# Performance work log

Hardware: AMD Instinct MI355X
Metric: run time of the kernel (lower is better)

The kernel has to match this reference:

```python
import jax, jax.numpy as jnp
import numpy as np

B, N, D_IN, D, H, L, NQ, NC, HID = 4, 25000, 32, 256, 8, 6, 100, 18, 1024


def _ln(x, g, b, eps=1e-5):
    m = jnp.mean(x, -1, keepdims=True)
    v = jnp.mean((x - m) ** 2, -1, keepdims=True)
    return (x - m) / jnp.sqrt(v + eps) * g + b


def _mha(q, kv, wqkv, bqkv, wo, bo, h):
    # q: (B, Lq, d), kv: (B, Lk, d); torch nn.MultiheadAttention math
    d = q.shape[-1]
    dh = d // h
    wq, wk, wv = jnp.split(wqkv, 3, axis=0)
    bq, bk, bv = jnp.split(bqkv, 3)
    Q = (q @ wq.T + bq).reshape(q.shape[0], q.shape[1], h, dh)
    K = (kv @ wk.T + bk).reshape(kv.shape[0], kv.shape[1], h, dh)
    V = (kv @ wv.T + bv).reshape(kv.shape[0], kv.shape[1], h, dh)
    s = jnp.einsum('bqhd,bkhd->bhqk', Q, K) / jnp.asarray(np.sqrt(dh), Q.dtype)
    a = jax.nn.softmax(s, axis=-1)
    o = jnp.einsum('bhqk,bkhd->bqhd', a, V).reshape(q.shape)
    return o @ wo.T + bo


def setup_inputs() -> dict:
    key = jax.random.key(0)
    ks = list(jax.random.split(key, 20))
    ki = iter(ks)

    def p(shape, s=0.02):
        return jax.random.normal(next(ki), shape, jnp.float32) * s

    inp = {
        'x': jax.random.normal(next(ki), (B * N, D_IN), jnp.float32),
        'batch_offsets': jnp.arange(B + 1, dtype=jnp.int32) * N,
        'ip_w': p((D, D_IN)), 'ip_b': jnp.zeros((D,), jnp.float32),
        'ip_ln_g': jnp.ones((D,), jnp.float32), 'ip_ln_b': jnp.zeros((D,), jnp.float32),
        'xm_w1': p((D, D_IN)), 'xm_b1': jnp.zeros((D,), jnp.float32),
        'xm_w2': p((D, D)), 'xm_b2': jnp.zeros((D,), jnp.float32),
        'query_embed': p((NQ, D), 1.0),
        'ca_wqkv': p((L, 3 * D, D)), 'ca_bqkv': jnp.zeros((L, 3 * D), jnp.float32),
        'ca_wo': p((L, D, D)), 'ca_bo': jnp.zeros((L, D), jnp.float32),
        'sa_wqkv': p((L, 3 * D, D)), 'sa_bqkv': jnp.zeros((L, 3 * D), jnp.float32),
        'sa_wo': p((L, D, D)), 'sa_bo': jnp.zeros((L, D), jnp.float32),
        'sa_ln_g': jnp.ones((L, D), jnp.float32), 'sa_ln_b': jnp.zeros((L, D), jnp.float32),
        'ffn_w1': p((L, HID, D)), 'ffn_b1': jnp.zeros((L, HID), jnp.float32),
        'ffn_w2': p((L, D, HID)), 'ffn_b2': jnp.zeros((L, D), jnp.float32),
        'ffn_ln_g': jnp.ones((L, D), jnp.float32), 'ffn_ln_b': jnp.zeros((L, D), jnp.float32),
        'out_ln_g': jnp.ones((D,), jnp.float32), 'out_ln_b': jnp.zeros((D,), jnp.float32),
        'cls_w1': p((D, D)), 'cls_b1': jnp.zeros((D,), jnp.float32),
        'cls_w2': p((NC + 1, D)), 'cls_b2': jnp.zeros((NC + 1,), jnp.float32),
    }
    return inp


def reference(x, batch_offsets, ip_w, ip_b, ip_ln_g, ip_ln_b, xm_w1, xm_b1, xm_w2, xm_b2,
              query_embed, ca_wqkv, ca_bqkv, ca_wo, ca_bo, sa_wqkv, sa_bqkv, sa_wo, sa_bo,
              sa_ln_g, sa_ln_b, ffn_w1, ffn_b1, ffn_w2, ffn_b2, ffn_ln_g, ffn_ln_b,
              out_ln_g, out_ln_b, cls_w1, cls_b1, cls_w2, cls_b2):
    b = batch_offsets.shape[0] - 1  # uniform segments -> batched attention
    n = x.shape[0] // b
    # input_proj: Linear -> LayerNorm -> ReLU
    inst = jax.nn.relu(_ln(x @ ip_w.T + ip_b, ip_ln_g, ip_ln_b)).reshape(b, n, -1)
    # x_mask: Linear -> ReLU -> Linear
    mask_feats = (jax.nn.relu(x @ xm_w1.T + xm_b1) @ xm_w2.T + xm_b2).reshape(b, n, -1)
    query = jnp.broadcast_to(query_embed, (b,) + query_embed.shape)
    for i in range(ca_wqkv.shape[0]):
        # CrossAttentionLayer: NOTE original discards dropout/norm results -> pure residual
        query = _mha(query, inst, ca_wqkv[i], ca_bqkv[i], ca_wo[i], ca_bo[i], H) + query
        # SelfAttentionLayer: residual + LayerNorm
        query = _ln(_mha(query, query, sa_wqkv[i], sa_bqkv[i], sa_wo[i], sa_bo[i], H) + query,
                    sa_ln_g[i], sa_ln_b[i])
        # FFN: residual + LayerNorm
        ff = jax.nn.relu(query @ ffn_w1[i].T + ffn_b1[i]) @ ffn_w2[i].T + ffn_b2[i]
        query = _ln(ff + query, ffn_ln_g[i], ffn_ln_b[i])
    qn = _ln(query, out_ln_g, out_ln_b)
    pred_labels = jax.nn.relu(qn @ cls_w1.T + cls_b1) @ cls_w2.T + cls_b2  # (b, NQ, NC+1)
    pred_masks = jnp.einsum('bqd,bnd->bqn', qn, mask_feats)  # (b, NQ, n)
    return pred_labels, pred_masks
```

## Files before the change

### kernel.cpp

```cpp
#include <hip/hip_runtime.h>

typedef unsigned short u16;
typedef unsigned int   u32;

constexpr int Bz   = 4;
constexpr int Ni   = 25000;
constexpr int BNi  = Bz * Ni;
constexpr int DIN  = 32;
constexpr int D    = 256;
constexpr int Hh   = 8;
constexpr int DH   = 32;
constexpr int Ll   = 6;
constexpr int NQ   = 100;
constexpr int NC1  = 19;
constexpr int HIDd = 1024;

constexpr int CHUNK  = 625;
constexpr int NCHUNK = Ni / CHUNK;
constexpr size_t PARTB = (size_t)Hh * NCHUNK * 128 * 34;
constexpr float SM_SCALE = 0.17677669529663687f;

__device__ __forceinline__ u16 f2b(float f) {
    union { float f; u32 u; } c; c.f = f;
    u32 u = c.u + 0x7FFFu + ((c.u >> 16) & 1u);
    return (u16)(u >> 16);
}

__global__ void k_cvt(const float* __restrict__ in, u16* __restrict__ out, int n) {
    for (int i = blockIdx.x * blockDim.x + threadIdx.x; i < n; i += gridDim.x * blockDim.x)
        out[i] = f2b(in[i]);
}

typedef __attribute__((ext_vector_type(8))) __bf16 bf8v;
typedef __attribute__((ext_vector_type(8))) short  s8v;
typedef __attribute__((ext_vector_type(4))) float  f4v;

template<bool DOLN>
__global__ __launch_bounds__(512) void k_inproj(
    const float* __restrict__ x, int row0, int Mloc,
    const u16* __restrict__ w16, const float* __restrict__ bias,
    const float* __restrict__ g, const float* __restrict__ bb,
    u16* __restrict__ outb)
{
    __shared__ u16 Ws[256 * 40];
    __shared__ float Cb[256], Cg[256], Cbb[256];
    const int tid = threadIdx.x, lane = tid & 63, w = tid >> 6;
    const int lr = lane & 15, hi = lane >> 4;

    for (int ch = tid; ch < 1024; ch += 512) {
        int r = ch >> 2, g4 = ch & 3;
        *(uint4*)&Ws[r * 40 + g4 * 8] = *(const uint4*)(w16 + r * 32 + g4 * 8);
    }
    if (tid < 256) {
        Cb[tid] = bias[tid];
        if (DOLN) { Cg[tid] = g[tid]; Cbb[tid] = bb[tid]; }
    }

    const int rloc = blockIdx.x * 128 + w * 16 + lr;
    const int gr = row0 + min(rloc, Mloc - 1);
    bf8v xf;
    {
        const float* xp = x + (size_t)gr * DIN + hi * 8;
        float4 a = *(const float4*)xp, c = *(const float4*)(xp + 4);
        union { s8v s; bf8v b; } u;
        u.s[0] = (short)f2b(a.x); u.s[1] = (short)f2b(a.y);
        u.s[2] = (short)f2b(a.z); u.s[3] = (short)f2b(a.w);
        u.s[4] = (short)f2b(c.x); u.s[5] = (short)f2b(c.y);
        u.s[6] = (short)f2b(c.z); u.s[7] = (short)f2b(c.w);
        xf = u.b;
    }
    __syncthreads();

    f4v acc[16];
    #pragma unroll
    for (int ci = 0; ci < 16; ci++) {
        acc[ci] = (f4v){0.f, 0.f, 0.f, 0.f};
        bf8v af = *(const bf8v*)&Ws[(ci * 16 + lr) * 40 + hi * 8];
        acc[ci] = __builtin_amdgcn_mfma_f32_16x16x32_bf16(af, xf, acc[ci], 0, 0, 0);
    }
    #pragma unroll
    for (int ci = 0; ci < 16; ci++)
        #pragma unroll
        for (int r = 0; r < 4; r++)
            acc[ci][r] += Cb[ci * 16 + hi * 4 + r];

    float mean = 0.f, ri = 1.f;
    if (DOLN) {
        float s = 0.f, q = 0.f;
        #pragma unroll
        for (int ci = 0; ci < 16; ci++)
            #pragma unroll
            for (int r = 0; r < 4; r++) { s += acc[ci][r]; q += acc[ci][r] * acc[ci][r]; }
        s += __shfl_xor(s, 16); s += __shfl_xor(s, 32);
        q += __shfl_xor(q, 16); q += __shfl_xor(q, 32);
        mean = s * (1.f / D);
        float var = q * (1.f / D) - mean * mean;
        ri = rsqrtf(var + 1e-5f);
    }
    if (rloc < Mloc) {
        #pragma unroll
        for (int ci = 0; ci < 16; ci++) {
            u16 o[4];
            #pragma unroll
            for (int r = 0; r < 4; r++) {
                float v = acc[ci][r];
                if (DOLN) v = (v - mean) * ri * Cg[ci * 16 + hi * 4 + r] + Cbb[ci * 16 + hi * 4 + r];
                o[r] = f2b(fmaxf(v, 0.f));
            }
            uint2 pk;
            pk.x = (u32)o[0] | ((u32)o[1] << 16);
            pk.y = (u32)o[2] | ((u32)o[3] << 16);
            *(uint2*)&outb[(size_t)rloc * 256 + ci * 16 + hi * 4] = pk;
        }
    }
}

__global__ __launch_bounds__(256) void k_ln(
    const float* __restrict__ in, float* __restrict__ out,
    const float* __restrict__ g, const float* __restrict__ b)
{
    const int t = threadIdx.x;
    const int row = blockIdx.x;
    float v = in[(size_t)row * D + t];
    float s = v, q = v * v;
    #pragma unroll
    for (int off = 32; off >= 1; off >>= 1) { s += __shfl_xor(s, off); q += __shfl_xor(q, off); }
    __shared__ float red[2][4];
    const int wid = t >> 6;
    if ((t & 63) == 0) { red[0][wid] = s; red[1][wid] = q; }
    __syncthreads();
    float S = red[0][0] + red[0][1] + red[0][2] + red[0][3];
    float Q = red[1][0] + red[1][1] + red[1][2] + red[1][3];
    float m   = S * (1.f / D);
    float var = Q * (1.f / D) - m * m;
    float ri  = rsqrtf(var + 1e-5f);
    out[(size_t)row * D + t] = (v - m) * ri * g[t] + b[t];
}

__global__ __launch_bounds__(256) void k_bcast(const float* __restrict__ qe, float* __restrict__ q)
{
    const int t = threadIdx.x;
    const int r = blockIdx.x;
    q[(size_t)r * D + t] = qe[(size_t)(r % NQ) * D + t];
}

template<int BM, int BN, int TM, int TN>
__global__ __launch_bounds__(256) void k_gemm(
    const float* __restrict__ A, const float* __restrict__ W,
    const float* __restrict__ bias, const float* __restrict__ resid,
    float* __restrict__ C, int M, int N, int K, int relu)
{
    constexpr int BK = 16;
    constexpr int TX = BN / TN, TY = BM / TM;
    static_assert(TX * TY == 256, "block must be 256 threads");
    __shared__ float As[BK][BM + 4];
    __shared__ float Ws[BK][BN + 4];

    const int tid = threadIdx.x;
    const int tx = tid % TX, ty = tid / TX;
    const int row0 = blockIdx.y * BM, col0 = blockIdx.x * BN;

    float acc[TM][TN];
    #pragma unroll
    for (int i = 0; i < TM; i++)
        #pragma unroll
        for (int j = 0; j < TN; j++) acc[i][j] = 0.f;

    for (int k0 = 0; k0 < K; k0 += BK) {
        __syncthreads();
        for (int idx = tid; idx < BM * (BK / 4); idx += 256) {
            int r = idx / (BK / 4), c4 = idx % (BK / 4);
            int gr = row0 + r;
            float4 v;
            if (gr < M) v = *(const float4*)(A + (size_t)gr * K + k0 + c4 * 4);
            else { v.x = v.y = v.z = v.w = 0.f; }
            As[c4*4+0][r] = v.x; As[c4*4+1][r] = v.y; As[c4*4+2][r] = v.z; As[c4*4+3][r] = v.w;
        }
        for (int idx = tid; idx < BN * (BK / 4); idx += 256) {
            int n = idx / (BK / 4), c4 = idx % (BK / 4);
            int gn = col0 + n;
            float4 v;
            if (gn < N) v = *(const float4*)(W + (size_t)gn * K + k0 + c4 * 4);
            else { v.x = v.y = v.z = v.w = 0.f; }
            Ws[c4*4+0][n] = v.x; Ws[c4*4+1][n] = v.y; Ws[c4*4+2][n] = v.z; Ws[c4*4+3][n] = v.w;
        }
        __syncthreads();
        #pragma unroll
        for (int kk = 0; kk < BK; kk++) {
            float a[TM], bb[TN];
            #pragma unroll
            for (int i = 0; i < TM; i++) a[i] = As[kk][ty * TM + i];
            #pragma unroll
            for (int j = 0; j < TN; j++) bb[j] = Ws[kk][tx * TN + j];
            #pragma unroll
            for (int i = 0; i < TM; i++)
                #pragma unroll
                for (int j = 0; j < TN; j++)
                    acc[i][j] = fmaf(a[i], bb[j], acc[i][j]);
        }
    }

    #pragma unroll
    for (int i = 0; i < TM; i++) {
        int gr = row0 + ty * TM + i;
        if (gr >= M) continue;
        #pragma unroll
        for (int j = 0; j < TN; j++) {
            int gn = col0 + tx * TN + j;
            if (gn >= N) continue;
            float v = acc[i][j];
            if (bias)  v += bias[gn];
            if (resid) v += resid[(size_t)gr * N + gn];
            if (relu)  v = fmaxf(v, 0.f);
            C[(size_t)gr * N + gn] = v;
        }
    }
}

template<bool RELU>
__global__ __launch_bounds__(256) void mm_small(
    const float* __restrict__ A, const u16* __restrict__ W,
    const float* __restrict__ bias, const float* __restrict__ resid,
    float* __restrict__ C, int M, int N, int K)
{
    __shared__ u16 As[64 * 40];
    __shared__ u16 Bs[64 * 40];
    const int tid  = threadIdx.x;
    const int lane = tid & 63, w = tid >> 6;
    const int wm = w >> 1, wn = w & 1;
    const int row0 = blockIdx.y * 64, col0 = blockIdx.x * 64;
    const int lr = lane & 15, hi = lane >> 4;

    f4v acc[2][2];
    #pragma unroll
    for (int i = 0; i < 2; i++)
        #pragma unroll
        for (int j = 0; j < 2; j++) acc[i][j] = (f4v){0.f, 0.f, 0.f, 0.f};

    const int sr = tid >> 2, sc = (tid & 3) * 8;
    const int ga = min(row0 + sr, M - 1);
    const int gw = min(col0 + sr, N - 1);

    for (int k0 = 0; k0 < K; k0 += 32) {
        __syncthreads();
        {
            const float* ap = A + (size_t)ga * K + k0 + sc;
            float4 a = *(const float4*)ap, c = *(const float4*)(ap + 4);
            union { s8v s; uint4 u; } cv;
            cv.s[0] = (short)f2b(a.x); cv.s[1] = (short)f2b(a.y);
            cv.s[2] = (short)f2b(a.z); cv.s[3] = (short)f2b(a.w);
            cv.s[4] = (short)f2b(c.x); cv.s[5] = (short)f2b(c.y);
            cv.s[6] = (short)f2b(c.z); cv.s[7] = (short)f2b(c.w);
            *(uint4*)&As[sr * 40 + sc] = cv.u;
            *(uint4*)&Bs[sr * 40 + sc] = *(const uint4*)(W + (size_t)gw * K + k0 + sc);
        }
        __syncthreads();
        bf8v a0 = *(const bf8v*)&As[(wm * 32      + lr) * 40 + hi * 8];
        bf8v a1 = *(const bf8v*)&As[(wm * 32 + 16 + lr) * 40 + hi * 8];
        bf8v b0 = *(const bf8v*)&Bs[(wn * 32      + lr) * 40 + hi * 8];
        bf8v b1 = *(const bf8v*)&Bs[(wn * 32 + 16 + lr) * 40 + hi * 8];
        acc[0][0] = __builtin_amdgcn_mfma_f32_16x16x32_bf16(a0, b0, acc[0][0], 0, 0, 0);
        acc[0][1] = __builtin_amdgcn_mfma_f32_16x16x32_bf16(a0, b1, acc[0][1], 0, 0, 0);
        acc[1][0] = __builtin_amdgcn_mfma_f32_16x16x32_bf16(a1, b0, acc[1][0], 0, 0, 0);
        acc[1][1] = __builtin_amdgcn_mfma_f32_16x16x32_bf16(a1, b1, acc[1][1], 0, 0, 0);
    }

    const int crl = hi * 4, ccl = lr;
    #pragma unroll
    for (int mi = 0; mi < 2; mi++)
        #pragma unroll
        for (int ni = 0; ni < 2; ni++)
            #pragma unroll
            for (int r = 0; r < 4; r++) {
                int grow = row0 + wm * 32 + mi * 16 + crl + r;
                int gcol = col0 + wn * 32 + ni * 16 + ccl;
                if (grow < M && gcol < N) {
                    float v = acc[mi][ni][r];
                    if (bias)  v += bias[gcol];
                    if (resid) v += resid[(size_t)grow * N + gcol];
                    if (RELU)  v = fmaxf(v, 0.f);
                    C[(size_t)grow * N + gcol] = v;
                }
            }
}

template<bool OUTBF>
__global__ __launch_bounds__(256) void mm128(
    const u16* __restrict__ A, const u16* __restrict__ W,
    const float* __restrict__ bias, void* __restrict__ Cv,
    int M, int N, int K, long long sA, long long sW, long long sC)
{
    __shared__ u16 As[128 * 40];
    __shared__ u16 Bs[128 * 40];
    A += (size_t)blockIdx.z * sA;
    W += (size_t)blockIdx.z * sW;
    const int tid = threadIdx.x, lane = tid & 63, w = tid >> 6;
    const int wm = w >> 1, wn = w & 1;
    const int row0 = blockIdx.y * 128, col0 = blockIdx.x * 128;
    const int lr = lane & 15, hi = lane >> 4;

    f4v acc[4][4];
    #pragma unroll
    for (int i = 0; i < 4; i++)
        #pragma unroll
        for (int j = 0; j < 4; j++) acc[i][j] = (f4v){0.f, 0.f, 0.f, 0.f};

    for (int k0 = 0; k0 < K; k0 += 32) {
        __syncthreads();
        #pragma unroll
        for (int i = 0; i < 2; i++) {
            int idx = tid + i * 256;
            int r = idx >> 2, kc = idx & 3;
            int ga = min(row0 + r, M - 1);
            int gb = min(col0 + r, N - 1);
            *(uint4*)&As[r * 40 + kc * 8] = *(const uint4*)(A + (size_t)ga * K + k0 + kc * 8);
            *(uint4*)&Bs[r * 40 + kc * 8] = *(const uint4*)(W + (size_t)gb * K + k0 + kc * 8);
        }
        __syncthreads();
        bf8v a[4], bb[4];
        #pragma unroll
        for (int mi = 0; mi < 4; mi++)
            a[mi] = *(const bf8v*)&As[(wm * 64 + mi * 16 + lr) * 40 + hi * 8];
        #pragma unroll
        for (int ni = 0; ni < 4; ni++)
            bb[ni] = *(const bf8v*)&Bs[(wn * 64 + ni * 16 + lr) * 40 + hi * 8];
        #pragma unroll
        for (int mi = 0; mi < 4; mi++)
            #pragma unroll
            for (int ni = 0; ni < 4; ni++)
                acc[mi][ni] = __builtin_amdgcn_mfma_f32_16x16x32_bf16(a[mi], bb[ni], acc[mi][ni], 0, 0, 0);
    }

    const int crl = hi * 4, ccl = lr;
    #pragma unroll
    for (int mi = 0; mi < 4; mi++)
        #pragma unroll
        for (int ni = 0; ni < 4; ni++)
            #pragma unroll
            for (int r = 0; r < 4; r++) {
                int grow = row0 + wm * 64 + mi * 16 + crl + r;
                int gcol = col0 + wn * 64 + ni * 16 + ccl;
                if (grow < M && gcol < N) {
                    float v = acc[mi][ni][r];
                    if (bias) v += bias[gcol];
                    if (OUTBF) ((u16*)Cv)[(size_t)blockIdx.z * sC + (size_t)grow * N + gcol] = f2b(v);
                    else       ((float*)Cv)[(size_t)blockIdx.z * sC + (size_t)grow * N + gcol] = v;
                }
            }
}

__global__ __launch_bounds__(512) void k_flash(
    const float* __restrict__ qbuf, const u16* __restrict__ kv,
    float* __restrict__ part, int bBase, size_t kvStride, size_t pStride)
{
    const int tid = threadIdx.x;
    const int lane = tid & 63, w = tid >> 6;
    const int h = blockIdx.y;
    const int b = bBase + blockIdx.z;
    const u16* kvp = kv + (size_t)blockIdx.z * kvStride;
    float* pp = part + (size_t)blockIdx.z * pStride;
    const int k0loc = blockIdx.x * CHUNK;
    const int lr = lane & 15, hi = lane >> 4;

    __shared__ u16 Ks[64 * 40];
    __shared__ u16 Vt[32 * 72];
    __shared__ u16 Pt[8][16 * 72];

    const int qt = w * 16 + lr;
    const int qg = b * NQ + min(qt, NQ - 1);
    bf8v qf;
    {
        const float* Qp = qbuf + (size_t)qg * D + h * DH + hi * 8;
        union { s8v s; bf8v b; } qu;
        #pragma unroll
        for (int j = 0; j < 8; j++) qu.s[j] = (short)f2b(Qp[j] * SM_SCALE);
        qf = qu.b;
    }

    float m = -1e30f, l = 0.f;
    f4v o0 = (f4v){0.f,0.f,0.f,0.f}, o1 = (f4v){0.f,0.f,0.f,0.f};

    constexpr int NSTEP = (CHUNK + 63) / 64;
    for (int s = 0; s < NSTEP; s++) {
        const int ck = k0loc + s * 64;
        const int nv = min(64, k0loc + CHUNK - ck);
        __syncthreads();
        if (tid < 256) {
            int key = tid >> 2, g = tid & 3;
            int krow = min(ck + key, Ni - 1);
            *(uint4*)&Ks[key * 40 + g * 8] =
                *(const uint4*)(kvp + (size_t)krow * (2 * D) + h * DH + g * 8);
        } else {
            int t2 = tid - 256;
            int key = t2 >> 2, g = t2 & 3;
            int krow = min(ck + key, Ni - 1);
            uint4 u = *(const uint4*)(kvp + (size_t)krow * (2 * D) + D + h * DH + g * 8);
            const u16* pu = (const u16*)&u;
            #pragma unroll
            for (int j = 0; j < 8; j++) Vt[(g * 8 + j) * 72 + key] = pu[j];
        }
        __syncthreads();

        f4v sf[4];
        #pragma unroll
        for (int j = 0; j < 4; j++) {
            bf8v kf = *(const bf8v*)&Ks[(j * 16 + lr) * 40 + hi * 8];
            sf[j] = (f4v){0.f,0.f,0.f,0.f};
            sf[j] = __builtin_amdgcn_mfma_f32_16x16x32_bf16(kf, qf, sf[j], 0, 0, 0);
        }

        float sv[16];
        #pragma unroll
        for (int j = 0; j < 4; j++)
            #pragma unroll
            for (int r = 0; r < 4; r++) {
                int key0 = j * 16 + hi * 4 + r;
                sv[j * 4 + r] = (key0 < nv) ? sf[j][r] : -1e30f;
            }
        float smax = sv[0];
        #pragma unroll
        for (int j = 1; j < 16; j++) smax = fmaxf(smax, sv[j]);
        smax = fmaxf(smax, __shfl_xor(smax, 16));
        smax = fmaxf(smax, __shfl_xor(smax, 32));
        float mnew  = fmaxf(m, smax);
        float scale = __expf(m - mnew);
        m = mnew;

        float psum = 0.f;
        u16 pb[16];
        #pragma unroll
        for (int j = 0; j < 16; j++) {
            float p = __expf(sv[j] - mnew);
            psum += p;
            pb[j] = f2b(p);
        }
        psum += __shfl_xor(psum, 16);
        psum += __shfl_xor(psum, 32);
        l = l * scale + psum;

        u16* pw = &Pt[w][lr * 72];
        #pragma unroll
        for (int j = 0; j < 4; j++) {
            *(u32*)&pw[j * 16 + hi * 4]     = (u32)pb[j*4+0] | ((u32)pb[j*4+1] << 16);
            *(u32*)&pw[j * 16 + hi * 4 + 2] = (u32)pb[j*4+2] | ((u32)pb[j*4+3] << 16);
        }

        const int qb4 = hi * 4;
        float f0 = __shfl(scale, qb4 + 0);
        float f1 = __shfl(scale, qb4 + 1);
        float f2 = __shfl(scale, qb4 + 2);
        float f3 = __shfl(scale, qb4 + 3);
        o0[0] *= f0; o0[1] *= f1; o0[2] *= f2; o0[3] *= f3;
        o1[0] *= f0; o1[1] *= f1; o1[2] *= f2; o1[3] *= f3;

        #pragma unroll
        for (int j = 0; j < 2; j++) {
            bf8v pf  = *(const bf8v*)&Pt[w][lr * 72 + j * 32 + hi * 8];
            bf8v vf0 = *(const bf8v*)&Vt[lr * 72 + j * 32 + hi * 8];
            bf8v vf1 = *(const bf8v*)&Vt[(16 + lr) * 72 + j * 32 + hi * 8];
            o0 = __builtin_amdgcn_mfma_f32_16x16x32_bf16(pf, vf0, o0, 0, 0, 0);
            o1 = __builtin_amdgcn_mfma_f32_16x16x32_bf16(pf, vf1, o1, 0, 0, 0);
        }
    }

    const size_t pbase = ((size_t)(h * NCHUNK + blockIdx.x) * 128) * 34;
    #pragma unroll
    for (int r = 0; r < 4; r++) {
        int qtr = w * 16 + hi * 4 + r;
        pp[pbase + (size_t)qtr * 34 + 2 + lr]      = o0[r];
        pp[pbase + (size_t)qtr * 34 + 2 + 16 + lr] = o1[r];
    }
    if (lane < 16) {
        pp[pbase + (size_t)(w * 16 + lane) * 34 + 0] = m;
        pp[pbase + (size_t)(w * 16 + lane) * 34 + 1] = l;
    }
}

__global__ __launch_bounds__(64) void k_fmerge(const float* __restrict__ part,
                                               float* __restrict__ abuf, int bBase, size_t pStride)
{
    const float* pz = part + (size_t)blockIdx.y * pStride;
    const int b = bBase + blockIdx.y;
    const int t = threadIdx.x;
    const int hq = blockIdx.x;
    const int h = hq / NQ, q = hq % NQ;
    float mmax = -1e30f;
    for (int c = 0; c < NCHUNK; c++)
        mmax = fmaxf(mmax, pz[((size_t)(h * NCHUNK + c) * 128 + q) * 34]);
    float L = 0.f, a = 0.f;
    for (int c = 0; c < NCHUNK; c++) {
        const float* p = &pz[((size_t)(h * NCHUNK + c) * 128 + q) * 34];
        float wv = __expf(p[0] - mmax);
        L += wv * p[1];
        if (t < DH) a += wv * p[2 + t];
    }
    if (t < DH)
        abuf[((size_t)(b * NQ + q)) * D + h * DH + t] = a / L;
}

__global__ __launch_bounds__(128) void k_sattn(const float* __restrict__ sqkv, float* __restrict__ abuf)
{
    const int tid = threadIdx.x;
    const int bh = blockIdx.x;
    const int b = bh >> 3, h = bh & 7;
    __shared__ float Ks[NQ][DH], Vs[NQ][DH];
    for (int idx = tid; idx < NQ * 8; idx += 128) {
        int kk = idx >> 3, f4 = idx & 7;
        const float* base = sqkv + ((size_t)(b * NQ + kk)) * (3 * D) + h * DH;
        *(float4*)&Ks[kk][f4 * 4] = *(const float4*)(base + D + f4 * 4);
        *(float4*)&Vs[kk][f4 * 4] = *(const float4*)(base + 2 * D + f4 * 4);
    }
    float qr[DH];
    const int q = tid;
    if (q < NQ) {
        const float* Qp = sqkv + ((size_t)(b * NQ + q)) * (3 * D) + h * DH;
        #pragma unroll
        for (int d = 0; d < DH; d += 4) {
            float4 v = *(const float4*)(Qp + d);
            qr[d] = v.x * SM_SCALE; qr[d+1] = v.y * SM_SCALE;
            qr[d+2] = v.z * SM_SCALE; qr[d+3] = v.w * SM_SCALE;
        }
    } else {
        #pragma unroll
        for (int d = 0; d < DH; d++) qr[d] = 0.f;
    }
    __syncthreads();
    float m = -1e30f, l = 0.f, acc[DH];
    #pragma unroll
    for (int d = 0; d < DH; d++) acc[d] = 0.f;
    for (int kk = 0; kk < NQ; kk++) {
        float sc = 0.f;
        #pragma unroll
        for (int d = 0; d < DH; d++) sc += qr[d] * Ks[kk][d];
        if (sc > m) {
            float r = __expf(m - sc);
            l *= r;
            #pragma unroll
            for (int d = 0; d < DH; d++) acc[d] *= r;
            m = sc;
        }
        float p = __expf(sc - m);
        l += p;
        #pragma unroll
        for (int d = 0; d < DH; d++) acc[d] += p * Vs[kk][d];
    }
    if (q < NQ) {
        float li = 1.f / l;
        float* o = abuf + ((size_t)(b * NQ + q)) * D + h * DH;
        #pragma unroll
        for (int d = 0; d < DH; d++) o[d] = acc[d] * li;
    }
}

extern "C" void kernel_launch(void* const* d_in, const int* in_sizes, int n_in,
                              void* d_out, int out_size, void* d_ws, size_t ws_size,
                              hipStream_t stream)
{
    const float* x        = (const float*)d_in[0];
    const float* ip_w     = (const float*)d_in[2];
    const float* ip_b     = (const float*)d_in[3];
    const float* ip_g     = (const float*)d_in[4];
    const float* ip_bb    = (const float*)d_in[5];
    const float* xm_w1    = (const float*)d_in[6];
    const float* xm_b1    = (const float*)d_in[7];
    const float* xm_w2    = (const float*)d_in[8];
    const float* xm_b2    = (const float*)d_in[9];
    const float* qe       = (const float*)d_in[10];
    const float* ca_wqkv  = (const float*)d_in[11];
    const float* ca_bqkv  = (const float*)d_in[12];
    const float* ca_wo    = (const float*)d_in[13];
    const float* ca_bo    = (const float*)d_in[14];
    const float* sa_wqkv  = (const float*)d_in[15];
    const float* sa_bqkv  = (const float*)d_in[16];
    const float* sa_wo    = (const float*)d_in[17];
    const float* sa_bo    = (const float*)d_in[18];
    const float* sa_ln_g  = (const float*)d_in[19];
    const float* sa_ln_b  = (const float*)d_in[20];
    const float* ffn_w1   = (const float*)d_in[21];
    const float* ffn_b1   = (const float*)d_in[22];
    const float* ffn_w2   = (const float*)d_in[23];
    const float* ffn_b2   = (const float*)d_in[24];
    const float* ffn_ln_g = (const float*)d_in[25];
    const float* ffn_ln_b = (const float*)d_in[26];
    const float* out_ln_g = (const float*)d_in[27];
    const float* out_ln_b = (const float*)d_in[28];
    const float* cls_w1   = (const float*)d_in[29];
    const float* cls_b1   = (const float*)d_in[30];
    const float* cls_w2   = (const float*)d_in[31];
    const float* cls_b2   = (const float*)d_in[32];
    float* out = (float*)d_out;

    bool batched = false;
    int instRows;
    if      (ws_size >= 210000000ull) { batched = true; instRows = BNi; }
    else if (ws_size >= 112000000ull) { instRows = BNi; }
    else if (ws_size >=  73000000ull) { instRows = Ni;  }
    else return;
    const bool instFull = (instRows == BNi);
    const int nzb = batched ? Bz : 1;

    char* wp = (char*)d_ws;
    auto alloc = [&](size_t bytes) -> char* {
        char* r = wp; wp += (bytes + 255) & ~(size_t)255; return r;
    };
    u16*   instb = (u16*)  alloc((size_t)instRows * D * 2);
    u16*   kvb   = (u16*)  alloc((size_t)(batched ? BNi : Ni) * 2 * D * 2);
    float* part  = (float*)alloc((size_t)nzb * PARTB * 4);
    float* qbuf  = (float*)alloc(409600);
    float* abuf  = (float*)alloc(409600);
    float* sqkv  = (float*)alloc(1228800);
    float* f1b   = (float*)alloc(1638400);
    float* qA    = (float*)alloc(409600);
    float* qB    = (float*)alloc(409600);
    u16*   ipw16 = (u16*)  alloc(256 * 32 * 2);
    u16*   xw116 = (u16*)  alloc(256 * 32 * 2);
    u16*   xw216 = (u16*)  alloc((size_t)D * D * 2);
    u16*   caq16 = (u16*)  alloc((size_t)Ll * 3 * D * D * 2);
    u16*   saq16 = (u16*)  alloc((size_t)Ll * 3 * D * D * 2);
    u16*   cao16 = (u16*)  alloc((size_t)Ll * D * D * 2);
    u16*   sao16 = (u16*)  alloc((size_t)Ll * D * D * 2);
    u16*   fw116 = (u16*)  alloc((size_t)Ll * HIDd * D * 2);
    u16*   fw216 = (u16*)  alloc((size_t)Ll * D * HIDd * 2);
    u16*   qnb   = (u16*)  alloc((size_t)Bz * NQ * D * 2);

    k_cvt<<<16,   256, 0, stream>>>(ip_w,  ipw16, 256 * 32);
    k_cvt<<<16,   256, 0, stream>>>(xm_w1, xw116, 256 * 32);
    k_cvt<<<64,   256, 0, stream>>>(xm_w2, xw216, D * D);
    k_cvt<<<1024, 256, 0, stream>>>(ca_wqkv, caq16, Ll * 3 * D * D);
    k_cvt<<<1024, 256, 0, stream>>>(sa_wqkv, saq16, Ll * 3 * D * D);
    k_cvt<<<512,  256, 0, stream>>>(ca_wo, cao16, Ll * D * D);
    k_cvt<<<512,  256, 0, stream>>>(sa_wo, sao16, Ll * D * D);
    k_cvt<<<1024, 256, 0, stream>>>(ffn_w1, fw116, Ll * HIDd * D);
    k_cvt<<<1024, 256, 0, stream>>>(ffn_w2, fw216, Ll * D * HIDd);

    if (instFull)
        k_inproj<true><<<(BNi + 127) / 128, 512, 0, stream>>>(
            x, 0, BNi, ipw16, ip_b, ip_g, ip_bb, instb);
    k_bcast<<<Bz * NQ, 256, 0, stream>>>(qe, qA);

    float* qcur = qA;
    float* qtmp = qB;
    for (int i = 0; i < Ll; i++) {
        const u16*   wq16 = caq16 + (size_t)i * 3 * D * D;
        const u16*   wkv16 = wq16 + (size_t)D * D;
        const float* bqkv = ca_bqkv + (size_t)i * 3 * D;
        mm_small<false><<<dim3(4, 7), 256, 0, stream>>>(
            qcur, wq16, bqkv, nullptr, qbuf, Bz * NQ, D, D);
        if (batched) {
            mm128<true><<<dim3(4, 196, 4), 256, 0, stream>>>(
                instb, wkv16, bqkv + D, kvb, Ni, 2 * D, D,
                (long long)Ni * D, 0, (long long)Ni * 2 * D);
            k_flash<<<dim3(NCHUNK, Hh, 4), 512, 0, stream>>>(
                qbuf, kvb, part, 0, (size_t)Ni * 2 * D, PARTB);
            k_fmerge<<<dim3(Hh * NQ, 4), 64, 0, stream>>>(part, abuf, 0, PARTB);
        } else {
            for (int b = 0; b < Bz; b++) {
                if (!instFull)
                    k_inproj<true><<<(Ni + 127) / 128, 512, 0, stream>>>(
                        x, b * Ni, Ni, ipw16, ip_b, ip_g, ip_bb, instb);
                const u16* ip = instFull ? instb + (size_t)b * Ni * D : instb;
                mm128<true><<<dim3(4, 196, 1), 256, 0, stream>>>(
                    ip, wkv16, bqkv + D, kvb, Ni, 2 * D, D, 0, 0, 0);
                k_flash<<<dim3(NCHUNK, Hh, 1), 512, 0, stream>>>(
                    qbuf, kvb, part, b, 0, 0);
                k_fmerge<<<dim3(Hh * NQ, 1), 64, 0, stream>>>(part, abuf, b, 0);
            }
        }
        mm_small<false><<<dim3(4, 7), 256, 0, stream>>>(
            abuf, cao16 + (size_t)i * D * D, ca_bo + (size_t)i * D, qcur, qtmp,
            Bz * NQ, D, D);
        { float* t2 = qcur; qcur = qtmp; qtmp = t2; }
        mm_small<false><<<dim3(12, 7), 256, 0, stream>>>(
            qcur, saq16 + (size_t)i * 3 * D * D, sa_bqkv + (size_t)i * 3 * D, nullptr, sqkv,
            Bz * NQ, 3 * D, D);
        k_sattn<<<Bz * Hh, 128, 0, stream>>>(sqkv, abuf);
        mm_small<false><<<dim3(4, 7), 256, 0, stream>>>(
            abuf, sao16 + (size_t)i * D * D, sa_bo + (size_t)i * D, qcur, qtmp,
            Bz * NQ, D, D);
        k_ln<<<Bz * NQ, 256, 0, stream>>>(qtmp, qtmp, sa_ln_g + i * D, sa_ln_b + i * D);
        { float* t2 = qcur; qcur = qtmp; qtmp = t2; }
        mm_small<true><<<dim3(16, 7), 256, 0, stream>>>(
            qcur, fw116 + (size_t)i * HIDd * D, ffn_b1 + (size_t)i * HIDd, nullptr, f1b,
            Bz * NQ, HIDd, D);
        mm_small<false><<<dim3(4, 7), 256, 0, stream>>>(
            f1b, fw216 + (size_t)i * D * HIDd, ffn_b2 + (size_t)i * D, qcur, qtmp,
            Bz * NQ, D, HIDd);
        k_ln<<<Bz * NQ, 256, 0, stream>>>(qtmp, qtmp, ffn_ln_g + i * D, ffn_ln_b + i * D);
        { float* t2 = qcur; qcur = qtmp; qtmp = t2; }
    }

    float* qn = qbuf;
    k_ln<<<Bz * NQ, 256, 0, stream>>>(qcur, qn, out_ln_g, out_ln_b);
    k_gemm<64,64,4,4><<<dim3(4, 7), 256, 0, stream>>>(
        qn, cls_w1, cls_b1, nullptr, abuf, Bz * NQ, D, D, 1);
    k_gemm<64,64,4,4><<<dim3(1, 7), 256, 0, stream>>>(
        abuf, cls_w2, cls_b2, nullptr, out, Bz * NQ, NC1, D, 0);

    k_cvt<<<128, 256, 0, stream>>>(qn, qnb, Bz * NQ * D);
    if (instFull) {
        k_inproj<false><<<(BNi + 127) / 128, 512, 0, stream>>>(
            x, 0, BNi, xw116, xm_b1, nullptr, nullptr, instb);
        if (batched) {
            mm128<true><<<dim3(2, 196, 4), 256, 0, stream>>>(
                instb, xw216, xm_b2, kvb, Ni, D, D,
                (long long)Ni * D, 0, (long long)Ni * D);
            mm128<false><<<dim3(196, 1, 4), 256, 0, stream>>>(
                qnb, kvb, nullptr, out + Bz * NQ * NC1, NQ, Ni, D,
                (long long)NQ * D, (long long)Ni * D, (long long)NQ * Ni);
        } else {
            for (int b = 0; b < Bz; b++) {
                mm128<true><<<dim3(2, 196, 1), 256, 0, stream>>>(
                    instb + (size_t)b * Ni * D, xw216, xm_b2, kvb, Ni, D, D, 0, 0, 0);
                mm128<false><<<dim3(196, 1, 1), 256, 0, stream>>>(
                    qnb + (size_t)b * NQ * D, kvb, nullptr,
                    out + Bz * NQ * NC1 + (size_t)b * NQ * Ni, NQ, Ni, D, 0, 0, 0);
            }
        }
    } else {
        for (int b = 0; b < Bz; b++) {
            k_inproj<false><<<(Ni + 127) / 128, 512, 0, stream>>>(
                x, b * Ni, Ni, xw116, xm_b1, nullptr, nullptr, instb);
            mm128<true><<<dim3(2, 196, 1), 256, 0, stream>>>(
                instb, xw216, xm_b2, kvb, Ni, D, D, 0, 0, 0);
            mm128<false><<<dim3(196, 1, 1), 256, 0, stream>>>(
                qnb + (size_t)b * NQ * D, kvb, nullptr,
                out + Bz * NQ * NC1 + (size_t)b * NQ * Ni, NQ, Ni, D, 0, 0, 0);
        }
    }
}
```

Baseline: 1.992 ms.

## Use direct global-to-LDS loads, XCD block swizzle, and staged bf16 stores in mm128

The mm128 GEMM that produces the cross-attention K/V now fills shared memory with global_load_lds (16-byte direct-to-LDS loads), so tiles no longer pass through registers. The unpadded LDS layout this requires may cause bank conflicts on the MFMA operand reads. Block indices are remapped so that consecutive tiles land on the same XCD, which is meant to improve L2 reuse. The bf16 output is staged through LDS in two halves and written with 16-byte coalesced stores instead of scattered 2-byte stores, at the cost of extra syncs.

Result: faster. 1.782 ms (-10.5%).

```diff
diff --git a/kernel.cpp b/kernel.cpp
--- a/kernel.cpp
+++ b/kernel.cpp
@@ -29,6 +29,12 @@
 __global__ void k_cvt(const float* __restrict__ in, u16* __restrict__ out, int n) {
     for (int i = blockIdx.x * blockDim.x + threadIdx.x; i < n; i += gridDim.x * blockDim.x)
         out[i] = f2b(in[i]);
+}
+
+__device__ __forceinline__ void gload16(const u16* g, u16* l) {
+    __builtin_amdgcn_global_load_lds(
+        (const __attribute__((address_space(1))) void*)g,
+        (__attribute__((address_space(3))) void*)l, 16, 0, 0);
 }
 
 typedef __attribute__((ext_vector_type(8))) __bf16 bf8v;
@@ -290,14 +296,25 @@
     const float* __restrict__ bias, void* __restrict__ Cv,
     int M, int N, int K, long long sA, long long sW, long long sC)
 {
-    __shared__ u16 As[128 * 40];
-    __shared__ u16 Bs[128 * 40];
-    A += (size_t)blockIdx.z * sA;
-    W += (size_t)blockIdx.z * sW;
+    __shared__ u16 sm[8192];
+    u16* As = sm;
+    u16* Bs = sm + 4096;
+
+    const int gx = gridDim.x, gy = gridDim.y;
+    const int total = gx * gy * (int)gridDim.z;
+    const int flat = blockIdx.x + gx * (blockIdx.y + gy * blockIdx.z);
+    const int q8 = total >> 3, r8 = total & 7;
+    const int xcd = flat & 7, blk = flat >> 3;
+    const int swz = (xcd < r8 ? xcd * (q8 + 1) : r8 * (q8 + 1) + (xcd - r8) * q8) + blk;
+    const int bx = swz % gx, by = (swz / gx) % gy, bz = swz / (gx * gy);
+
+    A += (size_t)bz * sA;
+    W += (size_t)bz * sW;
     const int tid = threadIdx.x, lane = tid & 63, w = tid >> 6;
     const int wm = w >> 1, wn = w & 1;
-    const int row0 = blockIdx.y * 128, col0 = blockIdx.x * 128;
+    const int row0 = by * 128, col0 = bx * 128;
     const int lr = lane & 15, hi = lane >> 4;
+    const int srow = lane >> 2, scol = (lane & 3) * 8;
 
     f4v acc[4][4];
     #pragma unroll
@@ -309,21 +326,21 @@
         __syncthreads();
         #pragma unroll
         for (int i = 0; i < 2; i++) {
-            int idx = tid + i * 256;
-            int r = idx >> 2, kc = idx & 3;
-            int ga = min(row0 + r, M - 1);
-            int gb = min(col0 + r, N - 1);
-            *(uint4*)&As[r * 40 + kc * 8] = *(const uint4*)(A + (size_t)ga * K + k0 + kc * 8);
-            *(uint4*)&Bs[r * 40 + kc * 8] = *(const uint4*)(W + (size_t)gb * K + k0 + kc * 8);
+            const int c = w * 2 + i;
+            const int row = c * 16 + srow;
+            const int gra = min(row0 + row, M - 1);
+            const int grb = min(col0 + row, N - 1);
+            gload16(A + (size_t)gra * K + k0 + scol, &As[c * 512]);
+            gload16(W + (size_t)grb * K + k0 + scol, &Bs[c * 512]);
         }
         __syncthreads();
         bf8v a[4], bb[4];
         #pragma unroll
         for (int mi = 0; mi < 4; mi++)
-            a[mi] = *(const bf8v*)&As[(wm * 64 + mi * 16 + lr) * 40 + hi * 8];
+            a[mi] = *(const bf8v*)&As[(wm * 64 + mi * 16 + lr) * 32 + hi * 8];
         #pragma unroll
         for (int ni = 0; ni < 4; ni++)
-            bb[ni] = *(const bf8v*)&Bs[(wn * 64 + ni * 16 + lr) * 40 + hi * 8];
+            bb[ni] = *(const bf8v*)&Bs[(wn * 64 + ni * 16 + lr) * 32 + hi * 8];
         #pragma unroll
         for (int mi = 0; mi < 4; mi++)
             #pragma unroll
@@ -331,22 +348,54 @@
                 acc[mi][ni] = __builtin_amdgcn_mfma_f32_16x16x32_bf16(a[mi], bb[ni], acc[mi][ni], 0, 0, 0);
     }
 
-    const int crl = hi * 4, ccl = lr;
-    #pragma unroll
-    for (int mi = 0; mi < 4; mi++)
-        #pragma unroll
-        for (int ni = 0; ni < 4; ni++)
-            #pragma unroll
-            for (int r = 0; r < 4; r++) {
-                int grow = row0 + wm * 64 + mi * 16 + crl + r;
-                int gcol = col0 + wn * 64 + ni * 16 + ccl;
-                if (grow < M && gcol < N) {
-                    float v = acc[mi][ni][r];
-                    if (bias) v += bias[gcol];
-                    if (OUTBF) ((u16*)Cv)[(size_t)blockIdx.z * sC + (size_t)grow * N + gcol] = f2b(v);
-                    else       ((float*)Cv)[(size_t)blockIdx.z * sC + (size_t)grow * N + gcol] = v;
+    if (OUTBF) {
+        #pragma unroll
+        for (int h0 = 0; h0 < 2; h0++) {
+            __syncthreads();
+            if (wm == h0) {
+                #pragma unroll
+                for (int mi = 0; mi < 4; mi++)
+                    #pragma unroll
+                    for (int ni = 0; ni < 4; ni++) {
+                        int gcol = col0 + wn * 64 + ni * 16 + lr;
+                        float bv = bias ? bias[gcol] : 0.f;
+                        #pragma unroll
+                        for (int r = 0; r < 4; r++) {
+                            int lrow = mi * 16 + hi * 4 + r;
+                            sm[lrow * 128 + wn * 64 + ni * 16 + lr] = f2b(acc[mi][ni][r] + bv);
+                        }
+                    }
+            }
+            __syncthreads();
+            u16* Cb16 = (u16*)Cv + (size_t)bz * sC;
+            #pragma unroll
+            for (int j = 0; j < 4; j++) {
+                int idx = tid + j * 256;
+                int lrow = idx >> 4, c16 = idx & 15;
+                int grow = row0 + h0 * 64 + lrow;
+                if (grow < M)
+                    *(uint4*)(Cb16 + (size_t)grow * N + col0 + c16 * 8) =
+                        *(const uint4*)&sm[lrow * 128 + c16 * 8];
+            }
+        }
+    } else {
+        const int crl = hi * 4, ccl = lr;
+        float* Cf = (float*)Cv + (size_t)bz * sC;
+        #pragma unroll
+        for (int mi = 0; mi < 4; mi++)
+            #pragma unroll
+            for (int ni = 0; ni < 4; ni++)
+                #pragma unroll
+                for (int r = 0; r < 4; r++) {
+                    int grow = row0 + wm * 64 + mi * 16 + crl + r;
+                    int gcol = col0 + wn * 64 + ni * 16 + ccl;
+                    if (grow < M && gcol < N) {
+                        float v = acc[mi][ni][r];
+                        if (bias) v += bias[gcol];
+                        Cf[(size_t)grow * N + gcol] = v;
+                    }
                 }
-            }
+    }
 }
 
 __global__ __launch_bounds__(512) void k_flash(
@@ -641,9 +690,9 @@
     float* qcur = qA;
     float* qtmp = qB;
     for (int i = 0; i < Ll; i++) {
-        const u16*   wq16 = caq16 + (size_t)i * 3 * D * D;
+        const u16*   wq16  = caq16 + (size_t)i * 3 * D * D;
         const u16*   wkv16 = wq16 + (size_t)D * D;
-        const float* bqkv = ca_bqkv + (size_t)i * 3 * D;
+        const float* bqkv  = ca_bqkv + (size_t)i * 3 * D;
         mm_small<false><<<dim3(4, 7), 256, 0, stream>>>(
             qcur, wq16, bqkv, nullptr, qbuf, Bz * NQ, D, D);
         if (batched) {
```
